# Kernel tuning notes

Hardware: AMD Instinct MI355X
Metric: run time of the kernel (lower is better)

## Reference

```python
import jax, jax.numpy as jnp
import numpy as np
from jax import lax


def setup_inputs() -> dict:
    key = jax.random.key(0)
    k1, k2 = jax.random.split(key)
    C, H, W = 64, 224, 224
    C_out, hf, wf = 128, 3, 3
    x = jax.random.normal(k1, (C, H, W), dtype=jnp.float32)
    kernels = jax.random.normal(k2, (C_out, C, hf, wf), dtype=jnp.float32)
    return {"x": x, "kernels": kernels}


def reference(x, kernels):
    # Original builds im2col columns per output pixel then does k_col @ x_col,
    # i.e. a cross-correlation with 'valid' padding and stride 1.
    # lax.conv_general_dilated computes exactly this (no kernel flip).
    stride = 1
    out = lax.conv_general_dilated(
        x[None],                       # (1, C, H, W) NCHW
        kernels,                       # (C_out, C_in, hf, wf) OIHW
        window_strides=(stride, stride),
        padding="VALID",
        dimension_numbers=("NCHW", "OIHW", "NCHW"),
    )
    return out[0]                      # (C_out, H_out, W_out)
```

## Files before the change

kernel.cpp:

```cpp
#include <hip/hip_runtime.h>
#include <hip/hip_bf16.h>


#define H_IN   224
#define W_IN   224
#define C_OUT  128
#define H_OUT  222
#define W_OUT  222
#define XP     226
#define CPAD   72
#define TW     68

typedef __attribute__((ext_vector_type(8)))  short bf16x8;
typedef __attribute__((ext_vector_type(16))) float f32x16;

static __device__ __forceinline__ unsigned short f2bs(float f) {
    union { __hip_bfloat16 h; unsigned short u; } cv;
    cv.h = __float2bfloat16(f);
    return cv.u;
}

__global__ __launch_bounds__(256)
void transform_w_kernel(const float* __restrict__ w, __hip_bfloat16* __restrict__ wt)
{
    int idx = blockIdx.x * 256 + threadIdx.x;
    if (idx < 9 * 128 * 64) {
        int ij  = idx >> 13;
        int rem = idx & 8191;
        int co  = rem >> 6;
        int c   = rem & 63;
        wt[((ij * 8 + (c >> 3)) * 128 + co) * 8 + (c & 7)] =
            __float2bfloat16(w[(co * 64 + c) * 9 + ij]);
    }
}

__global__ __launch_bounds__(256)
void transpose_x_kernel(const float* __restrict__ x, __hip_bfloat16* __restrict__ xt)
{
    __shared__ __align__(16) unsigned short tile[64 * TW];
    const int h  = blockIdx.y;
    const int w0 = blockIdx.x * 64;
    const int t  = threadIdx.x;

    {
        const int wq = (t & 15) * 4;
        const int c0 = t >> 4;
        #pragma unroll
        for (int p = 0; p < 4; ++p) {
            const int c  = c0 + p * 16;
            const int wg = w0 + wq;
            float4 v = make_float4(0.f, 0.f, 0.f, 0.f);
            if (h < H_IN && wg < W_IN)
                v = *(const float4*)(x + ((size_t)c * H_IN + h) * W_IN + wg);
            ushort4 b;
            b.x = f2bs(v.x); b.y = f2bs(v.y); b.z = f2bs(v.z); b.w = f2bs(v.w);
            *(ushort4*)(tile + c * TW + wq) = b;
        }
    }
    __syncthreads();

    {
        const int wl = t >> 2;
        const int cq = (t & 3) * 16;
        const int wg = w0 + wl;
        if (wg < XP) {
            alignas(16) unsigned short r[16];
            #pragma unroll
            for (int k = 0; k < 16; ++k)
                r[k] = tile[(cq + k) * TW + wl];
            float4* d = (float4*)((unsigned short*)xt + ((size_t)h * XP + wg) * 64 + cq);
            d[0] = ((const float4*)r)[0];
            d[1] = ((const float4*)r)[1];
        }
    }
}

__global__ __launch_bounds__(256, 4)
void conv_mfma_kernel(const __hip_bfloat16* __restrict__ xt,
                      const __hip_bfloat16* __restrict__ wt,
                      float* __restrict__ out)
{
    __shared__ __hip_bfloat16 xs[6 * 34 * CPAD];
    const int ow0 = blockIdx.x * 32;
    const int oh0 = blockIdx.y * 4;
    const int co0 = blockIdx.z * 64;
    const int tid = threadIdx.x;

    for (int q = tid; q < 6 * 34 * 8; q += 256) {
        int sub = q & 7;
        int pix = q >> 3;
        int row = pix / 34;
        int wc  = pix - row * 34;
        *(float4*)(xs + (row * 34 + wc) * CPAD + sub * 8) =
            *(const float4*)(xt + ((oh0 + row) * XP + (ow0 + wc)) * 64 + sub * 8);
    }
    __syncthreads();

    const int wave = tid >> 6;
    const int lane = tid & 63;
    const int n    = lane & 31;
    const int h    = lane >> 5;

    f32x16 acc[2] = {};

    #pragma unroll
    for (int p = 0; p < 9; ++p) {
        const int i  = p / 3;
        const int jj = p - i * 3;
        #pragma unroll
        for (int t = 0; t < 4; ++t) {
            bf16x8 afr[2];
            #pragma unroll
            for (int mi = 0; mi < 2; ++mi)
                afr[mi] = *(const bf16x8*)(wt +
                    (size_t)(((p * 8 + t * 2 + h) * 128 + co0 + mi * 32 + n) * 8));
            bf16x8 bfr = *(const bf16x8*)(xs +
                ((i + wave) * 34 + n + jj) * CPAD + t * 16 + h * 8);
            #pragma unroll
            for (int mi = 0; mi < 2; ++mi)
                acc[mi] = __builtin_amdgcn_mfma_f32_32x32x16_bf16(
                    afr[mi], bfr, acc[mi], 0, 0, 0);
        }
    }

    const int oh = oh0 + wave;
    const int ow = ow0 + n;
    if (oh < H_OUT && ow < W_OUT) {
        #pragma unroll
        for (int mi = 0; mi < 2; ++mi) {
            #pragma unroll
            for (int r = 0; r < 16; ++r) {
                int co = co0 + mi * 32 + (r & 3) + 8 * (r >> 2) + 4 * h;
                out[(size_t)co * (H_OUT * W_OUT) + oh * W_OUT + ow] = acc[mi][r];
            }
        }
    }
}

extern "C" void kernel_launch(void* const* d_in, const int* in_sizes, int n_in,
                              void* d_out, int out_size, void* d_ws, size_t ws_size,
                              hipStream_t stream)
{
    const float* x = (const float*)d_in[0];
    const float* w = (const float*)d_in[1];
    float* out     = (float*)d_out;

    __hip_bfloat16* xt = (__hip_bfloat16*)d_ws;
    __hip_bfloat16* wt = (__hip_bfloat16*)((char*)d_ws + (size_t)XP * XP * 64 * 2);

    transform_w_kernel<<<288, 256, 0, stream>>>(w, wt);
    transpose_x_kernel<<<dim3(4, XP), 256, 0, stream>>>(x, xt);
    conv_mfma_kernel<<<dim3(7, 56, 2), 256, 0, stream>>>(xt, wt, out);
}
```

Baseline: 88.01 us.

## Merge prep kernels and give each conv wave two output rows

Fuses the weight transform and the input transpose into one launch, dispatching on block index, which removes one kernel launch. The conv kernel now runs 2 waves per block instead of 4, and each wave computes two output rows with a 2x2 MFMA accumulator tile. Each weight fragment loaded from global memory is therefore reused across two rows, halving weight fragment traffic per output. In exchange each wave holds twice the accumulator registers and each block has fewer threads to do the shared-memory fill.

```diff
diff --git a/kernel.cpp b/kernel.cpp
--- a/kernel.cpp
+++ b/kernel.cpp
@@ -11,6 +11,9 @@
 #define CPAD   72
 #define TW     68
 
+#define PREP_W_UNITS 288
+#define PREP_UNITS   1192
+
 typedef __attribute__((ext_vector_type(8)))  short bf16x8;
 typedef __attribute__((ext_vector_type(16))) float f32x16;
 
@@ -21,26 +24,27 @@
 }
 
 __global__ __launch_bounds__(256)
-void transform_w_kernel(const float* __restrict__ w, __hip_bfloat16* __restrict__ wt)
+void prep_kernel(const float* __restrict__ x, const float* __restrict__ w,
+                 __hip_bfloat16* __restrict__ xt, __hip_bfloat16* __restrict__ wt)
 {
-    int idx = blockIdx.x * 256 + threadIdx.x;
-    if (idx < 9 * 128 * 64) {
+    __shared__ __align__(16) unsigned short tile[64 * TW];
+    const int u = blockIdx.x;
+    const int t = threadIdx.x;
+
+    if (u < PREP_W_UNITS) {
+        int idx = u * 256 + t;
         int ij  = idx >> 13;
         int rem = idx & 8191;
         int co  = rem >> 6;
         int c   = rem & 63;
         wt[((ij * 8 + (c >> 3)) * 128 + co) * 8 + (c & 7)] =
             __float2bfloat16(w[(co * 64 + c) * 9 + ij]);
+        return;
     }
-}
 
-__global__ __launch_bounds__(256)
-void transpose_x_kernel(const float* __restrict__ x, __hip_bfloat16* __restrict__ xt)
-{
-    __shared__ __align__(16) unsigned short tile[64 * TW];
-    const int h  = blockIdx.y;
-    const int w0 = blockIdx.x * 64;
-    const int t  = threadIdx.x;
+    const int ux = u - PREP_W_UNITS;
+    const int h  = ux >> 2;
+    const int w0 = (ux & 3) * 64;
 
     {
         const int wq = (t & 15) * 4;
@@ -75,7 +79,7 @@
     }
 }
 
-__global__ __launch_bounds__(256, 4)
+__global__ __launch_bounds__(128, 2)
 void conv_mfma_kernel(const __hip_bfloat16* __restrict__ xt,
                       const __hip_bfloat16* __restrict__ wt,
                       float* __restrict__ out)
@@ -86,7 +90,7 @@
     const int co0 = blockIdx.z * 64;
     const int tid = threadIdx.x;
 
-    for (int q = tid; q < 6 * 34 * 8; q += 256) {
+    for (int q = tid; q < 6 * 34 * 8; q += 128) {
         int sub = q & 7;
         int pix = q >> 3;
         int row = pix / 34;
@@ -100,8 +104,9 @@
     const int lane = tid & 63;
     const int n    = lane & 31;
     const int h    = lane >> 5;
+    const int r0   = wave * 2;
 
-    f32x16 acc[2] = {};
+    f32x16 acc[2][2] = {};
 
     #pragma unroll
     for (int p = 0; p < 9; ++p) {
@@ -109,29 +114,36 @@
         const int jj = p - i * 3;
         #pragma unroll
         for (int t = 0; t < 4; ++t) {
-            bf16x8 afr[2];
+            bf16x8 afr[2], bfr[2];
             #pragma unroll
             for (int mi = 0; mi < 2; ++mi)
                 afr[mi] = *(const bf16x8*)(wt +
                     (size_t)(((p * 8 + t * 2 + h) * 128 + co0 + mi * 32 + n) * 8));
-            bf16x8 bfr = *(const bf16x8*)(xs +
-                ((i + wave) * 34 + n + jj) * CPAD + t * 16 + h * 8);
+            #pragma unroll
+            for (int ni = 0; ni < 2; ++ni)
+                bfr[ni] = *(const bf16x8*)(xs +
+                    ((i + r0 + ni) * 34 + n + jj) * CPAD + t * 16 + h * 8);
             #pragma unroll
             for (int mi = 0; mi < 2; ++mi)
-                acc[mi] = __builtin_amdgcn_mfma_f32_32x32x16_bf16(
-                    afr[mi], bfr, acc[mi], 0, 0, 0);
+                #pragma unroll
+                for (int ni = 0; ni < 2; ++ni)
+                    acc[mi][ni] = __builtin_amdgcn_mfma_f32_32x32x16_bf16(
+                        afr[mi], bfr[ni], acc[mi][ni], 0, 0, 0);
         }
     }
 
-    const int oh = oh0 + wave;
-    const int ow = ow0 + n;
-    if (oh < H_OUT && ow < W_OUT) {
+    #pragma unroll
+    for (int mi = 0; mi < 2; ++mi) {
         #pragma unroll
-        for (int mi = 0; mi < 2; ++mi) {
-            #pragma unroll
-            for (int r = 0; r < 16; ++r) {
-                int co = co0 + mi * 32 + (r & 3) + 8 * (r >> 2) + 4 * h;
-                out[(size_t)co * (H_OUT * W_OUT) + oh * W_OUT + ow] = acc[mi][r];
+        for (int ni = 0; ni < 2; ++ni) {
+            const int oh = oh0 + r0 + ni;
+            const int ow = ow0 + n;
+            if (oh < H_OUT && ow < W_OUT) {
+                #pragma unroll
+                for (int r = 0; r < 16; ++r) {
+                    int co = co0 + mi * 32 + (r & 3) + 8 * (r >> 2) + 4 * h;
+                    out[(size_t)co * (H_OUT * W_OUT) + oh * W_OUT + ow] = acc[mi][ni][r];
+                }
             }
         }
     }
@@ -148,7 +160,6 @@
     __hip_bfloat16* xt = (__hip_bfloat16*)d_ws;
     __hip_bfloat16* wt = (__hip_bfloat16*)((char*)d_ws + (size_t)XP * XP * 64 * 2);
 
-    transform_w_kernel<<<288, 256, 0, stream>>>(w, wt);
-    transpose_x_kernel<<<dim3(4, XP), 256, 0, stream>>>(x, xt);
-    conv_mfma_kernel<<<dim3(7, 56, 2), 256, 0, stream>>>(xt, wt, out);
+    prep_kernel<<<PREP_UNITS, 256, 0, stream>>>(x, w, xt, wt);
+    conv_mfma_kernel<<<dim3(7, 56, 2), 128, 0, stream>>>(xt, wt, out);
 }
```

Measured after the change: 88.39 us. About the same (+0.4%).
